# Kernel optimization log

Hardware: AMD Instinct MI355X
Metric: run time of the kernel (lower is better)

The kernel has to match this reference:

```python
import jax, jax.numpy as jnp
import numpy as np

B, N, F = 8, 1024, 256
OUT, REL = 256, 16
NADJ = 7  # ((2 relations + consecutive) * 2 for backward) + self link


def setup_inputs() -> dict:
    key = jax.random.key(0)
    k0, k1, k2, k3, k4 = jax.random.split(key, 5)
    features = jax.random.normal(k0, (B, N, F), dtype=jnp.float32)
    A1 = jax.random.uniform(k1, (B, N, N), dtype=jnp.float32)
    A2 = jax.random.uniform(k2, (B, N, N), dtype=jnp.float32)
    # learned params: one (F+REL, OUT) weight per adjacency matrix, edge embeddings init 'ones', bias (N, OUT)
    W = jax.random.normal(k3, (NADJ, F + REL, OUT), dtype=jnp.float32) * 0.05
    W_edges = jnp.ones((NADJ, REL), dtype=jnp.float32)
    b = jax.random.uniform(k4, (N, OUT), dtype=jnp.float32, minval=-0.05, maxval=0.05)
    return {"features": features, "A1": A1, "A2": A2, "W": W, "W_edges": W_edges, "b": b}


def reference(features, A1, A2, W, W_edges, b):
    # eye = A[0] * zeros(N) + eye(N)  -> batch-broadcast identity [B,N,N]
    eye = jnp.zeros_like(A1) + jnp.eye(N, dtype=A1.dtype)
    # original rolls along axis 0 (batch) of the broadcast identity (faithful replication)
    shifted = jnp.roll(eye, 1, axis=0)
    A_fwd = [A1, A2, shifted]                      # relations + consecutive link
    A_list = A_fwd + [jnp.swapaxes(a, 1, 2) for a in A_fwd]  # backward links
    A_list.append(eye)                             # self links
    A = jnp.stack(A_list, axis=0)                  # [R,B,N,N]

    # concat(features, tile(W_edges[r])) @ W[r] == features @ W[r][:F] + W_edges[r] @ W[r][F:]
    HW = jnp.einsum('bnf,rfo->rbno', features, W[:, :F]) \
         + jnp.einsum('rd,rdo->ro', W_edges, W[:, F:])[:, None, None, :]  # [R,B,N,OUT]
    AHW = jnp.einsum('rbnm,rbmo->rbno', A, HW)     # batched adjacency matmul
    out = jnp.max(AHW, axis=0) + b                 # max-aggregate over relations, add bias
    return out                                     # activation = linear
```

## Files before the change

kernel.cpp:

```cpp
#include <hip/hip_runtime.h>
#include <hip/hip_bf16.h>

#define B_ 8
#define N_ 1024
#define F_ 256
#define OUT_ 256
#define REL_ 16
#define NADJ_ 7

typedef __attribute__((ext_vector_type(8))) _Float16 f16x8;
typedef __attribute__((ext_vector_type(4))) float f32x4;

__device__ __forceinline__ void gll16(const _Float16* g, _Float16* l) {
    __builtin_amdgcn_global_load_lds(
        (const __attribute__((address_space(1))) void*)g,
        (__attribute__((address_space(3))) void*)l, 16, 0, 0);
}

__constant__ const int c_perm[7] = {0, 1, 3, 4, 2, 5, 6};

__global__ __launch_bounds__(256) void prep_kernel(const float* __restrict__ W,
                                                   const float* __restrict__ We,
                                                   const float* __restrict__ feat,
                                                   float* __restrict__ cb,
                                                   _Float16* __restrict__ WTp,
                                                   _Float16* __restrict__ Fe) {
    int bid = blockIdx.x, tid = threadIdx.x;
    if (bid < 7) {
        int idx = bid * 256 + tid;
        int j = idx / OUT_, o = idx % OUT_;
        int r = c_perm[j];
        const float* Wr = W + (size_t)r * (F_ + REL_) * OUT_;
        float s = 0.f;
#pragma unroll
        for (int d = 0; d < REL_; ++d) s += We[r * REL_ + d] * Wr[(F_ + d) * OUT_ + o];
        cb[idx] = s;
    } else if (bid < 1799) {
        int idx = (bid - 7) * 256 + tid;
        int j = idx >> 16, rem = idx & 65535, o = rem >> 8, f = rem & 255;
        int r = c_perm[j];
        WTp[idx] = (_Float16)W[((size_t)r * (F_ + REL_) + f) * OUT_ + o];
    } else {
        int i = (bid - 1799) * 256 + tid;
        size_t base = (size_t)i * 8;
        float4 a = *(const float4*)(feat + base);
        float4 b = *(const float4*)(feat + base + 4);
        f16x8 v = {(_Float16)a.x, (_Float16)a.y, (_Float16)a.z, (_Float16)a.w,
                   (_Float16)b.x, (_Float16)b.y, (_Float16)b.z, (_Float16)b.w};
        *(f16x8*)(Fe + base) = v;
    }
}

__global__ __launch_bounds__(256) void convhw_kernel(const float* __restrict__ A1,
                                                     const float* __restrict__ A2,
                                                     const _Float16* __restrict__ Fe,
                                                     const _Float16* __restrict__ WTp,
                                                     const float* __restrict__ cb,
                                                     _Float16* __restrict__ Af,
                                                     _Float16* __restrict__ HWT,
                                                     _Float16* __restrict__ HWN) {
    __shared__ _Float16 S[8192];
    const int bid = blockIdx.x, tid = threadIdx.x;
    if (bid < 896) {
        const int z = bid / 128, rem = bid % 128, bx = rem & 63, by = rem >> 6;
        const bool tr = (z < 4);
        const _Float16* A  = tr ? (WTp + (size_t)z * 65536) : Fe;
        const _Float16* Bt = tr ? Fe : (WTp + (size_t)z * 65536);
        const int m0 = (tr ? by : bx) * 128;
        const int n0 = (tr ? bx : by) * 128;
        _Float16* As = S;
        _Float16* Bs = S + 4096;
        const int wave = tid >> 6, lane = tid & 63, lm = lane & 15, q = lane >> 4;
        const int wr = (wave >> 1) * 64, wc = (wave & 1) * 64;
        const int srow = tid >> 2, sk = (tid & 3) * 8;
        const _Float16* ga0 = A + (size_t)(m0 + srow) * F_ + sk;
        const _Float16* ga1 = ga0 + (size_t)64 * F_;
        const _Float16* gb0 = Bt + (size_t)(n0 + srow) * F_ + sk;
        const _Float16* gb1 = gb0 + (size_t)64 * F_;
        _Float16* la0 = As + tid * 8;
        _Float16* la1 = As + 2048 + tid * 8;
        _Float16* lb0 = Bs + tid * 8;
        _Float16* lb1 = Bs + 2048 + tid * 8;

        f32x4 acc[4][4] = {};
        for (int k0 = 0; k0 < F_; k0 += 32) {
            gll16(ga0 + k0, la0);
            gll16(ga1 + k0, la1);
            gll16(gb0 + k0, lb0);
            gll16(gb1 + k0, lb1);
            __syncthreads();
            f16x8 af[4], bf[4];
#pragma unroll
            for (int i = 0; i < 4; ++i) af[i] = *(const f16x8*)(As + (wr + i * 16 + lm) * 32 + q * 8);
#pragma unroll
            for (int j = 0; j < 4; ++j) bf[j] = *(const f16x8*)(Bs + (wc + j * 16 + lm) * 32 + q * 8);
#pragma unroll
            for (int i = 0; i < 4; ++i)
#pragma unroll
                for (int j = 0; j < 4; ++j)
                    acc[i][j] = __builtin_amdgcn_mfma_f32_16x16x32_f16(af[i], bf[j], acc[i][j], 0, 0, 0);
            __syncthreads();
        }
        const float* cbz = cb + (size_t)z * 256;
        if (tr) {
            _Float16* C = HWT + (size_t)z * ((size_t)256 * 8192);
#pragma unroll
            for (int i = 0; i < 4; ++i)
#pragma unroll
                for (int j = 0; j < 4; ++j)
#pragma unroll
                    for (int g = 0; g < 4; ++g) {
                        int row = wr + i * 16 + q * 4 + g;
                        int col = wc + j * 16 + lm;
                        float v = acc[i][j][g] + cbz[m0 + row];
                        C[(size_t)(m0 + row) * 8192 + (n0 + col)] = (_Float16)v;
                    }
        } else {
            _Float16* C = HWN + (size_t)(z - 4) * ((size_t)8192 * 256);
#pragma unroll
            for (int i = 0; i < 4; ++i)
#pragma unroll
                for (int j = 0; j < 4; ++j)
#pragma unroll
                    for (int g = 0; g < 4; ++g) {
                        int row = wr + i * 16 + q * 4 + g;
                        int col = wc + j * 16 + lm;
                        float v = acc[i][j][g] + cbz[n0 + col];
                        C[(size_t)(m0 + row) * 256 + (n0 + col)] = (_Float16)v;
                    }
        }
    } else {
        _Float16* T = S;
        const int cbid = bid - 896;
        int z = cbid >> 8, s = z >> 3, b = z & 7;
        const float* src = (s ? A2 : A1) + (size_t)b * N_ * N_;
        int k0 = (cbid & 15) * 64, n0 = ((cbid >> 4) & 15) * 64;
        int r = tid >> 2, cs = (tid & 3) * 16;
        const float* sp = src + (size_t)(k0 + r) * N_ + n0 + cs;
        _Float16 v[16];
#pragma unroll
        for (int j = 0; j < 16; j += 4) {
            float4 f = *(const float4*)(sp + j);
            v[j] = (_Float16)f.x; v[j + 1] = (_Float16)f.y;
            v[j + 2] = (_Float16)f.z; v[j + 3] = (_Float16)f.w;
        }
        const size_t slab = (size_t)8 * N_ * N_;
#pragma unroll
        for (int j = 0; j < 16; ++j) {
            int n = cs + j;
            int sw = ((n ^ (n >> 3)) & 7) << 3;
            T[n * 64 + (r ^ sw)] = v[j];
        }
        __syncthreads();
        {
            int n = tid >> 2, i2 = (tid & 3) * 16;
            int sw = ((n ^ (n >> 3)) & 7) << 3;
            f16x8 q0 = *(const f16x8*)&T[n * 64 + (i2 ^ sw)];
            f16x8 q1 = *(const f16x8*)&T[n * 64 + ((i2 + 8) ^ sw)];
            _Float16* dt = Af + (size_t)s * slab + (size_t)b * N_ * N_ + (size_t)(n0 + n) * N_ + k0 + i2;
            *(f16x8*)dt = q0;
            *(f16x8*)(dt + 8) = q1;
        }
    }
}

__global__ __launch_bounds__(256) void p2_kernel(const float* __restrict__ A1,
                                                 const float* __restrict__ A2,
                                                 const _Float16* __restrict__ Af,
                                                 const _Float16* __restrict__ HWT,
                                                 _Float16* __restrict__ AHW) {
    __shared__ _Float16 As[128 * 32];
    __shared__ _Float16 Bs[128 * 32];
    const int d = blockIdx.x;
    const int member = (d >> 3) & 1;
    const int p = (d & 7) | ((d >> 4) << 3);
    const int mt = p & 7, zz = p >> 3;
    const int rr = zz >> 3, b = zz & 7;
    const _Float16* Bt = HWT + (size_t)rr * (256 * 8192) + (size_t)b * 1024;
    _Float16* C = AHW + (size_t)rr * (8 * 262144) + (size_t)b * 262144;
    const int m0 = mt * 128, n0 = member * 128;
    const int tid = threadIdx.x;
    const int wave = tid >> 6, lane = tid & 63, lm = lane & 15, q = lane >> 4;
    const int wr = (wave >> 1) * 64, wc = (wave & 1) * 64;
    const int srow = tid >> 2, sk = (tid & 3) * 8;
    const _Float16* gb0 = Bt + (size_t)(n0 + srow) * 8192 + sk;
    const _Float16* gb1 = gb0 + (size_t)64 * 8192;
    _Float16* la0 = As + tid * 8;
    _Float16* la1 = As + 2048 + tid * 8;
    _Float16* lb0 = Bs + tid * 8;
    _Float16* lb1 = Bs + 2048 + tid * 8;

    f32x4 acc[4][4] = {};
    if (rr < 2) {
        const float* Ag0 = ((rr & 1) ? A2 : A1) + (size_t)b * N_ * N_
                           + (size_t)(m0 + srow) * N_ + sk;
        const float* Ag1 = Ag0 + (size_t)64 * N_;
        float4 pa0 = *(const float4*)(Ag0);
        float4 pa1 = *(const float4*)(Ag0 + 4);
        float4 pb0 = *(const float4*)(Ag1);
        float4 pb1 = *(const float4*)(Ag1 + 4);
        for (int k0 = 0; k0 < N_; k0 += 32) {
            f16x8 v0 = {(_Float16)pa0.x, (_Float16)pa0.y, (_Float16)pa0.z, (_Float16)pa0.w,
                        (_Float16)pa1.x, (_Float16)pa1.y, (_Float16)pa1.z, (_Float16)pa1.w};
            f16x8 v1 = {(_Float16)pb0.x, (_Float16)pb0.y, (_Float16)pb0.z, (_Float16)pb0.w,
                        (_Float16)pb1.x, (_Float16)pb1.y, (_Float16)pb1.z, (_Float16)pb1.w};
            *(f16x8*)la0 = v0;
            *(f16x8*)la1 = v1;
            gll16(gb0 + k0, lb0);
            gll16(gb1 + k0, lb1);
            if (k0 + 32 < N_) {
                pa0 = *(const float4*)(Ag0 + k0 + 32);
                pa1 = *(const float4*)(Ag0 + k0 + 36);
                pb0 = *(const float4*)(Ag1 + k0 + 32);
                pb1 = *(const float4*)(Ag1 + k0 + 36);
            }
            __syncthreads();
            f16x8 af[4], bf[4];
#pragma unroll
            for (int i = 0; i < 4; ++i) af[i] = *(const f16x8*)(As + (wr + i * 16 + lm) * 32 + q * 8);
#pragma unroll
            for (int j = 0; j < 4; ++j) bf[j] = *(const f16x8*)(Bs + (wc + j * 16 + lm) * 32 + q * 8);
#pragma unroll
            for (int i = 0; i < 4; ++i)
#pragma unroll
                for (int j = 0; j < 4; ++j)
                    acc[i][j] = __builtin_amdgcn_mfma_f32_16x16x32_f16(af[i], bf[j], acc[i][j], 0, 0, 0);
            __syncthreads();
        }
    } else {
        const _Float16* ga0 = Af + (size_t)(rr - 2) * (8 * 1048576) + (size_t)b * 1048576
                              + (size_t)(m0 + srow) * N_ + sk;
        const _Float16* ga1 = ga0 + (size_t)64 * N_;
        for (int k0 = 0; k0 < N_; k0 += 32) {
            gll16(ga0 + k0, la0);
            gll16(ga1 + k0, la1);
            gll16(gb0 + k0, lb0);
            gll16(gb1 + k0, lb1);
            __syncthreads();
            f16x8 af[4], bf[4];
#pragma unroll
            for (int i = 0; i < 4; ++i) af[i] = *(const f16x8*)(As + (wr + i * 16 + lm) * 32 + q * 8);
#pragma unroll
            for (int j = 0; j < 4; ++j) bf[j] = *(const f16x8*)(Bs + (wc + j * 16 + lm) * 32 + q * 8);
#pragma unroll
            for (int i = 0; i < 4; ++i)
#pragma unroll
                for (int j = 0; j < 4; ++j)
                    acc[i][j] = __builtin_amdgcn_mfma_f32_16x16x32_f16(af[i], bf[j], acc[i][j], 0, 0, 0);
            __syncthreads();
        }
    }
#pragma unroll
    for (int i = 0; i < 4; ++i)
#pragma unroll
        for (int j = 0; j < 4; ++j)
#pragma unroll
            for (int g = 0; g < 4; ++g) {
                int row = wr + i * 16 + q * 4 + g;
                int col = wc + j * 16 + lm;
                C[(size_t)(m0 + row) * 256 + (n0 + col)] = (_Float16)acc[i][j][g];
            }
}

__global__ __launch_bounds__(256) void max_kernel(const _Float16* __restrict__ AHW,
                                                  const _Float16* __restrict__ HWN,
                                                  const float* __restrict__ bias,
                                                  float* __restrict__ out) {
    size_t i = ((size_t)blockIdx.x * 256 + threadIdx.x) * 8;
    const size_t slab = (size_t)B_ * N_ * OUT_;
    float m[8];
    f16x8 v = *(const f16x8*)(AHW + i);
#pragma unroll
    for (int e = 0; e < 8; ++e) m[e] = (float)v[e];
#pragma unroll
    for (int rr = 1; rr < 4; ++rr) {
        f16x8 w = *(const f16x8*)(AHW + rr * slab + i);
#pragma unroll
        for (int e = 0; e < 8; ++e) m[e] = fmaxf(m[e], (float)w[e]);
    }
#pragma unroll
    for (int j = 0; j < 3; ++j) {
        f16x8 w = *(const f16x8*)(HWN + j * slab + i);
#pragma unroll
        for (int e = 0; e < 8; ++e) m[e] = fmaxf(m[e], (float)w[e]);
    }
    size_t bidx = i & ((size_t)N_ * OUT_ - 1);
    float4 b0 = *(const float4*)(bias + bidx);
    float4 b1 = *(const float4*)(bias + bidx + 4);
    float4 o0 = {m[0] + b0.x, m[1] + b0.y, m[2] + b0.z, m[3] + b0.w};
    float4 o1 = {m[4] + b1.x, m[5] + b1.y, m[6] + b1.z, m[7] + b1.w};
    *(float4*)(out + i) = o0;
    *(float4*)(out + i + 4) = o1;
}

__global__ void cbias_kernel(const float* __restrict__ W, const float* __restrict__ We,
                             float* __restrict__ c) {
    int idx = blockIdx.x * 256 + threadIdx.x;
    if (idx >= NADJ_ * OUT_) return;
    int r = idx / OUT_, o = idx % OUT_;
    const float* Wr = W + (size_t)r * (F_ + REL_) * OUT_;
    float s = 0.f;
#pragma unroll
    for (int d = 0; d < REL_; ++d) s += We[r * REL_ + d] * Wr[(F_ + d) * OUT_ + o];
    c[idx] = s;
}

__global__ __launch_bounds__(256) void hw_kernel(const float* __restrict__ feat,
                                                 const float* __restrict__ W,
                                                 const float* __restrict__ cb,
                                                 _Float16* __restrict__ HWb) {
    __shared__ _Float16 As[64][32];
    __shared__ _Float16 Bs[64][32];
    const int mt = blockIdx.x, ct = blockIdx.y;
    const int tid = threadIdx.x, wave = tid >> 6, lane = tid & 63;
    const int r = (ct * 64) / OUT_;
    const int o0 = (ct * 64) % OUT_;
    const float* Bg = W + (size_t)r * (F_ + REL_) * OUT_ + o0;
    const int m0 = mt * 64;
    const int lm = lane & 15, q = lane >> 4;
    f32x4 acc[4] = {};
    for (int k0 = 0; k0 < F_; k0 += 32) {
        {
            int seg = (tid & 3) * 8, m = tid >> 2;
            const float* src = feat + (size_t)(m0 + m) * F_ + k0 + seg;
#pragma unroll
            for (int j = 0; j < 8; ++j) As[m][seg + j] = (_Float16)src[j];
        }
        {
            int kk = tid >> 3, ns = (tid & 7) * 8;
            const float* src = Bg + (size_t)(k0 + kk) * OUT_ + ns;
#pragma unroll
            for (int j = 0; j < 8; ++j) Bs[ns + j][kk] = (_Float16)src[j];
        }
        __syncthreads();
        f16x8 a = *(const f16x8*)&As[wave * 16 + lm][q * 8];
#pragma unroll
        for (int c4 = 0; c4 < 4; ++c4) {
            f16x8 b = *(const f16x8*)&Bs[c4 * 16 + lm][q * 8];
            acc[c4] = __builtin_amdgcn_mfma_f32_16x16x32_f16(a, b, acc[c4], 0, 0, 0);
        }
        __syncthreads();
    }
#pragma unroll
    for (int c4 = 0; c4 < 4; ++c4)
#pragma unroll
        for (int g = 0; g < 4; ++g) {
            int row = wave * 16 + (lane >> 4) * 4 + g;
            int col = c4 * 16 + lm;
            float v = acc[c4][g] + cb[r * OUT_ + o0 + col];
            HWb[((size_t)r * B_ * N_ + m0 + row) * OUT_ + o0 + col] = (_Float16)v;
        }
}

__global__ __launch_bounds__(256) void agg_kernel(const float* __restrict__ A1,
                                                  const float* __restrict__ A2,
                                                  const _Float16* __restrict__ HWb,
                                                  const float* __restrict__ bias,
                                                  float* __restrict__ out) {
    __shared__ _Float16 As[64][32];
    __shared__ _Float16 Bs[64][32];
    const int b = blockIdx.z, nt = blockIdx.y, ot = blockIdx.x;
    const int tid = threadIdx.x, wave = tid >> 6, lane = tid & 63;
    const int n0 = nt * 64, o0 = ot * 64;
    const int lm = lane & 15, q = lane >> 4;
    const size_t rstride = (size_t)B_ * N_ * OUT_;
    f32x4 mx[4];
#pragma unroll
    for (int i = 0; i < 4; ++i) mx[i] = f32x4{-1e30f, -1e30f, -1e30f, -1e30f};
#pragma unroll 1
    for (int rr = 0; rr < 4; ++rr) {
        const float* Ag = ((rr & 1) ? A2 : A1) + (size_t)b * N_ * N_;
        const bool tr = (rr >= 2);
        const int r = (rr < 2) ? rr : rr + 1;
        const _Float16* Bg = HWb + (size_t)r * rstride + (size_t)b * N_ * OUT_ + o0;
        f32x4 acc[4] = {};
        for (int k0 = 0; k0 < N_; k0 += 32) {
            if (!tr) {
                int seg = (tid & 3) * 8, m = tid >> 2;
                const float* src = Ag + (size_t)(n0 + m) * N_ + k0 + seg;
#pragma unroll
                for (int j = 0; j < 8; ++j) As[m][seg + j] = (_Float16)src[j];
            } else {
                int kk = tid >> 3, ms = (tid & 7) * 8;
                const float* src = Ag + (size_t)(k0 + kk) * N_ + n0 + ms;
#pragma unroll
                for (int j = 0; j < 8; ++j) As[ms + j][kk] = (_Float16)src[j];
            }
            {
                int kk = tid >> 3, ns = (tid & 7) * 8;
                const _Float16* src = Bg + (size_t)(k0 + kk) * OUT_ + ns;
#pragma unroll
                for (int j = 0; j < 8; ++j) Bs[ns + j][kk] = src[j];
            }
            __syncthreads();
            f16x8 a = *(const f16x8*)&As[wave * 16 + lm][q * 8];
#pragma unroll
            for (int c4 = 0; c4 < 4; ++c4) {
                f16x8 bb = *(const f16x8*)&Bs[c4 * 16 + lm][q * 8];
                acc[c4] = __builtin_amdgcn_mfma_f32_16x16x32_f16(a, bb, acc[c4], 0, 0, 0);
            }
            __syncthreads();
        }
#pragma unroll
        for (int c4 = 0; c4 < 4; ++c4)
#pragma unroll
            for (int g = 0; g < 4; ++g) mx[c4][g] = fmaxf(mx[c4][g], acc[c4][g]);
    }
#pragma unroll
    for (int c4 = 0; c4 < 4; ++c4)
#pragma unroll
        for (int g = 0; g < 4; ++g) {
            int row = wave * 16 + (lane >> 4) * 4 + g;
            int col = c4 * 16 + lm;
            size_t pos = ((size_t)b * N_ + n0 + row) * OUT_ + o0 + col;
            float v = mx[c4][g];
            v = fmaxf(v, (float)HWb[2 * rstride + pos]);
            v = fmaxf(v, (float)HWb[5 * rstride + pos]);
            v = fmaxf(v, (float)HWb[6 * rstride + pos]);
            out[pos] = v + bias[((size_t)(n0 + row)) * OUT_ + o0 + col];
        }
}

extern "C" void kernel_launch(void* const* d_in, const int* in_sizes, int n_in,
                              void* d_out, int out_size, void* d_ws, size_t ws_size,
                              hipStream_t stream) {
    const float* feat = (const float*)d_in[0];
    const float* A1   = (const float*)d_in[1];
    const float* A2   = (const float*)d_in[2];
    const float* W    = (const float*)d_in[3];
    const float* We   = (const float*)d_in[4];
    const float* bias = (const float*)d_in[5];
    float* out = (float*)d_out;

    const size_t OFF_CB   = 0;
    const size_t OFF_WT   = 8192;
    const size_t OFF_FE   = 1048576;
    const size_t OFF_AF   = 5242880;
    const size_t OFF_HWT  = 72351744;
    const size_t OFF_HWN  = 89128960;
    const size_t OFF_AHW  = 101711872;
    const size_t WS_NEEDED = 118489088;

    if (ws_size >= WS_NEEDED) {
        float*    cbp = (float*)((char*)d_ws + OFF_CB);
        _Float16* WTp = (_Float16*)((char*)d_ws + OFF_WT);
        _Float16* Fe  = (_Float16*)((char*)d_ws + OFF_FE);
        _Float16* Af  = (_Float16*)((char*)d_ws + OFF_AF);
        _Float16* HWT = (_Float16*)((char*)d_ws + OFF_HWT);
        _Float16* HWN = (_Float16*)((char*)d_ws + OFF_HWN);
        _Float16* AHW = (_Float16*)((char*)d_ws + OFF_AHW);

        prep_kernel<<<2823, 256, 0, stream>>>(W, We, feat, cbp, WTp, Fe);
        convhw_kernel<<<4992, 256, 0, stream>>>(A1, A2, Fe, WTp, cbp, Af, HWT, HWN);
        p2_kernel<<<512, 256, 0, stream>>>(A1, A2, Af, HWT, AHW);
        max_kernel<<<1024, 256, 0, stream>>>(AHW, HWN, bias, out);
    } else {
        float* cb = (float*)d_ws;
        _Float16* HWb = (_Float16*)((char*)d_ws + 8192);
        cbias_kernel<<<7, 256, 0, stream>>>(W, We, cb);
        hw_kernel<<<dim3(128, 28), 256, 0, stream>>>(feat, W, cb, HWb);
        agg_kernel<<<dim3(4, 16, 8), 256, 0, stream>>>(A1, A2, HWb, bias, out);
    }
}
```

Before: 176.4 us.

## Fuse A transpose-to-fp16 into aggregation GEMM, dropping Af staging buffer

Removes the separate pass that converted A1/A2 to fp16 and transposed them into a workspace buffer. The aggregation kernel now reads fp32 A directly, transposes it on the fly into an XOR-swizzled shared-memory tile, and prefetches the next k-slice into registers. The forward-A path gets the same swizzle. This avoids writing and re-reading 32 MB of fp16 A. In exchange, the transposed reads are fp32 and column-strided, and each output tile re-reads and re-converts A instead of reading pre-converted fp16.

```diff
diff --git a/kernel.cpp b/kernel.cpp
--- a/kernel.cpp
+++ b/kernel.cpp
@@ -9,6 +9,7 @@
 #define NADJ_ 7
 
 typedef __attribute__((ext_vector_type(8))) _Float16 f16x8;
+typedef __attribute__((ext_vector_type(2))) _Float16 f16x2;
 typedef __attribute__((ext_vector_type(4))) float f32x4;
 
 __device__ __forceinline__ void gll16(const _Float16* g, _Float16* l) {
@@ -51,122 +52,83 @@
     }
 }
 
-__global__ __launch_bounds__(256) void convhw_kernel(const float* __restrict__ A1,
-                                                     const float* __restrict__ A2,
-                                                     const _Float16* __restrict__ Fe,
-                                                     const _Float16* __restrict__ WTp,
-                                                     const float* __restrict__ cb,
-                                                     _Float16* __restrict__ Af,
-                                                     _Float16* __restrict__ HWT,
-                                                     _Float16* __restrict__ HWN) {
-    __shared__ _Float16 S[8192];
-    const int bid = blockIdx.x, tid = threadIdx.x;
-    if (bid < 896) {
-        const int z = bid / 128, rem = bid % 128, bx = rem & 63, by = rem >> 6;
-        const bool tr = (z < 4);
-        const _Float16* A  = tr ? (WTp + (size_t)z * 65536) : Fe;
-        const _Float16* Bt = tr ? Fe : (WTp + (size_t)z * 65536);
-        const int m0 = (tr ? by : bx) * 128;
-        const int n0 = (tr ? bx : by) * 128;
-        _Float16* As = S;
-        _Float16* Bs = S + 4096;
-        const int wave = tid >> 6, lane = tid & 63, lm = lane & 15, q = lane >> 4;
-        const int wr = (wave >> 1) * 64, wc = (wave & 1) * 64;
-        const int srow = tid >> 2, sk = (tid & 3) * 8;
-        const _Float16* ga0 = A + (size_t)(m0 + srow) * F_ + sk;
-        const _Float16* ga1 = ga0 + (size_t)64 * F_;
-        const _Float16* gb0 = Bt + (size_t)(n0 + srow) * F_ + sk;
-        const _Float16* gb1 = gb0 + (size_t)64 * F_;
-        _Float16* la0 = As + tid * 8;
-        _Float16* la1 = As + 2048 + tid * 8;
-        _Float16* lb0 = Bs + tid * 8;
-        _Float16* lb1 = Bs + 2048 + tid * 8;
-
-        f32x4 acc[4][4] = {};
-        for (int k0 = 0; k0 < F_; k0 += 32) {
-            gll16(ga0 + k0, la0);
-            gll16(ga1 + k0, la1);
-            gll16(gb0 + k0, lb0);
-            gll16(gb1 + k0, lb1);
-            __syncthreads();
-            f16x8 af[4], bf[4];
-#pragma unroll
-            for (int i = 0; i < 4; ++i) af[i] = *(const f16x8*)(As + (wr + i * 16 + lm) * 32 + q * 8);
-#pragma unroll
-            for (int j = 0; j < 4; ++j) bf[j] = *(const f16x8*)(Bs + (wc + j * 16 + lm) * 32 + q * 8);
-#pragma unroll
-            for (int i = 0; i < 4; ++i)
-#pragma unroll
-                for (int j = 0; j < 4; ++j)
-                    acc[i][j] = __builtin_amdgcn_mfma_f32_16x16x32_f16(af[i], bf[j], acc[i][j], 0, 0, 0);
-            __syncthreads();
-        }
-        const float* cbz = cb + (size_t)z * 256;
-        if (tr) {
-            _Float16* C = HWT + (size_t)z * ((size_t)256 * 8192);
-#pragma unroll
-            for (int i = 0; i < 4; ++i)
-#pragma unroll
-                for (int j = 0; j < 4; ++j)
-#pragma unroll
-                    for (int g = 0; g < 4; ++g) {
-                        int row = wr + i * 16 + q * 4 + g;
-                        int col = wc + j * 16 + lm;
-                        float v = acc[i][j][g] + cbz[m0 + row];
-                        C[(size_t)(m0 + row) * 8192 + (n0 + col)] = (_Float16)v;
-                    }
-        } else {
-            _Float16* C = HWN + (size_t)(z - 4) * ((size_t)8192 * 256);
-#pragma unroll
-            for (int i = 0; i < 4; ++i)
-#pragma unroll
-                for (int j = 0; j < 4; ++j)
-#pragma unroll
-                    for (int g = 0; g < 4; ++g) {
-                        int row = wr + i * 16 + q * 4 + g;
-                        int col = wc + j * 16 + lm;
-                        float v = acc[i][j][g] + cbz[n0 + col];
-                        C[(size_t)(m0 + row) * 256 + (n0 + col)] = (_Float16)v;
-                    }
-        }
+__global__ __launch_bounds__(256) void hw7_kernel(const _Float16* __restrict__ Fe,
+                                                  const _Float16* __restrict__ WTp,
+                                                  const float* __restrict__ cb,
+                                                  _Float16* __restrict__ HWT,
+                                                  _Float16* __restrict__ HWN) {
+    __shared__ _Float16 As[128 * 32];
+    __shared__ _Float16 Bs[128 * 32];
+    const int z = blockIdx.z, bx = blockIdx.x, by = blockIdx.y;
+    const bool tr = (z < 4);
+    const _Float16* A  = tr ? (WTp + (size_t)z * 65536) : Fe;
+    const _Float16* Bt = tr ? Fe : (WTp + (size_t)z * 65536);
+    const int m0 = (tr ? by : bx) * 128;
+    const int n0 = (tr ? bx : by) * 128;
+    const int tid = threadIdx.x;
+    const int wave = tid >> 6, lane = tid & 63, lm = lane & 15, q = lane >> 4;
+    const int wr = (wave >> 1) * 64, wc = (wave & 1) * 64;
+    const int srow = tid >> 2, sk = (tid & 3) * 8;
+    const _Float16* ga0 = A + (size_t)(m0 + srow) * F_ + sk;
+    const _Float16* ga1 = ga0 + (size_t)64 * F_;
+    const _Float16* gb0 = Bt + (size_t)(n0 + srow) * F_ + sk;
+    const _Float16* gb1 = gb0 + (size_t)64 * F_;
+    _Float16* la0 = As + tid * 8;
+    _Float16* la1 = As + 2048 + tid * 8;
+    _Float16* lb0 = Bs + tid * 8;
+    _Float16* lb1 = Bs + 2048 + tid * 8;
+
+    f32x4 acc[4][4] = {};
+    for (int k0 = 0; k0 < F_; k0 += 32) {
+        gll16(ga0 + k0, la0);
+        gll16(ga1 + k0, la1);
+        gll16(gb0 + k0, lb0);
+        gll16(gb1 + k0, lb1);
+        __syncthreads();
+        f16x8 af[4], bf[4];
+#pragma unroll
+        for (int i = 0; i < 4; ++i) af[i] = *(const f16x8*)(As + (wr + i * 16 + lm) * 32 + q * 8);
+#pragma unroll
+        for (int j = 0; j < 4; ++j) bf[j] = *(const f16x8*)(Bs + (wc + j * 16 + lm) * 32 + q * 8);
+#pragma unroll
+        for (int i = 0; i < 4; ++i)
+#pragma unroll
+            for (int j = 0; j < 4; ++j)
+                acc[i][j] = __builtin_amdgcn_mfma_f32_16x16x32_f16(af[i], bf[j], acc[i][j], 0, 0, 0);
+        __syncthreads();
+    }
+    const float* cbz = cb + (size_t)z * 256;
+    if (tr) {
+        _Float16* C = HWT + (size_t)z * ((size_t)256 * 8192);
+#pragma unroll
+        for (int i = 0; i < 4; ++i)
+#pragma unroll
+            for (int j = 0; j < 4; ++j)
+#pragma unroll
+                for (int g = 0; g < 4; ++g) {
+                    int row = wr + i * 16 + q * 4 + g;
+                    int col = wc + j * 16 + lm;
+                    float v = acc[i][j][g] + cbz[m0 + row];
+                    C[(size_t)(m0 + row) * 8192 + (n0 + col)] = (_Float16)v;
+                }
     } else {
-        _Float16* T = S;
-        const int cbid = bid - 896;
-        int z = cbid >> 8, s = z >> 3, b = z & 7;
-        const float* src = (s ? A2 : A1) + (size_t)b * N_ * N_;
-        int k0 = (cbid & 15) * 64, n0 = ((cbid >> 4) & 15) * 64;
-        int r = tid >> 2, cs = (tid & 3) * 16;
-        const float* sp = src + (size_t)(k0 + r) * N_ + n0 + cs;
-        _Float16 v[16];
-#pragma unroll
-        for (int j = 0; j < 16; j += 4) {
-            float4 f = *(const float4*)(sp + j);
-            v[j] = (_Float16)f.x; v[j + 1] = (_Float16)f.y;
-            v[j + 2] = (_Float16)f.z; v[j + 3] = (_Float16)f.w;
-        }
-        const size_t slab = (size_t)8 * N_ * N_;
-#pragma unroll
-        for (int j = 0; j < 16; ++j) {
-            int n = cs + j;
-            int sw = ((n ^ (n >> 3)) & 7) << 3;
-            T[n * 64 + (r ^ sw)] = v[j];
-        }
-        __syncthreads();
-        {
-            int n = tid >> 2, i2 = (tid & 3) * 16;
-            int sw = ((n ^ (n >> 3)) & 7) << 3;
-            f16x8 q0 = *(const f16x8*)&T[n * 64 + (i2 ^ sw)];
-            f16x8 q1 = *(const f16x8*)&T[n * 64 + ((i2 + 8) ^ sw)];
-            _Float16* dt = Af + (size_t)s * slab + (size_t)b * N_ * N_ + (size_t)(n0 + n) * N_ + k0 + i2;
-            *(f16x8*)dt = q0;
-            *(f16x8*)(dt + 8) = q1;
-        }
+        _Float16* C = HWN + (size_t)(z - 4) * ((size_t)8192 * 256);
+#pragma unroll
+        for (int i = 0; i < 4; ++i)
+#pragma unroll
+            for (int j = 0; j < 4; ++j)
+#pragma unroll
+                for (int g = 0; g < 4; ++g) {
+                    int row = wr + i * 16 + q * 4 + g;
+                    int col = wc + j * 16 + lm;
+                    float v = acc[i][j][g] + cbz[n0 + col];
+                    C[(size_t)(m0 + row) * 256 + (n0 + col)] = (_Float16)v;
+                }
     }
 }
 
 __global__ __launch_bounds__(256) void p2_kernel(const float* __restrict__ A1,
                                                  const float* __restrict__ A2,
-                                                 const _Float16* __restrict__ Af,
                                                  const _Float16* __restrict__ HWT,
                                                  _Float16* __restrict__ AHW) {
     __shared__ _Float16 As[128 * 32];
@@ -185,15 +147,16 @@
     const int srow = tid >> 2, sk = (tid & 3) * 8;
     const _Float16* gb0 = Bt + (size_t)(n0 + srow) * 8192 + sk;
     const _Float16* gb1 = gb0 + (size_t)64 * 8192;
-    _Float16* la0 = As + tid * 8;
-    _Float16* la1 = As + 2048 + tid * 8;
     _Float16* lb0 = Bs + tid * 8;
     _Float16* lb1 = Bs + 2048 + tid * 8;
-
+    const int swA = (q * 8) ^ ((lm & 3) << 3);
+
+    const float* Ag = ((rr & 1) ? A2 : A1) + (size_t)b * N_ * N_;
     f32x4 acc[4][4] = {};
     if (rr < 2) {
-        const float* Ag0 = ((rr & 1) ? A2 : A1) + (size_t)b * N_ * N_
-                           + (size_t)(m0 + srow) * N_ + sk;
+        _Float16* la0 = As + srow * 32 + (sk ^ ((srow & 3) << 3));
+        _Float16* la1 = la0 + 64 * 32;
+        const float* Ag0 = Ag + (size_t)(m0 + srow) * N_ + sk;
         const float* Ag1 = Ag0 + (size_t)64 * N_;
         float4 pa0 = *(const float4*)(Ag0);
         float4 pa1 = *(const float4*)(Ag0 + 4);
@@ -217,9 +180,11 @@
             __syncthreads();
             f16x8 af[4], bf[4];
 #pragma unroll
-            for (int i = 0; i < 4; ++i) af[i] = *(const f16x8*)(As + (wr + i * 16 + lm) * 32 + q * 8);
-#pragma unroll
-            for (int j = 0; j < 4; ++j) bf[j] = *(const f16x8*)(Bs + (wc + j * 16 + lm) * 32 + q * 8);
+            for (int i = 0; i < 4; ++i)
+                af[i] = *(const f16x8*)(As + (wr + i * 16 + lm) * 32 + swA);
+#pragma unroll
+            for (int j = 0; j < 4; ++j)
+                bf[j] = *(const f16x8*)(Bs + (wc + j * 16 + lm) * 32 + q * 8);
 #pragma unroll
             for (int i = 0; i < 4; ++i)
 #pragma unroll
@@ -228,20 +193,37 @@
             __syncthreads();
         }
     } else {
-        const _Float16* ga0 = Af + (size_t)(rr - 2) * (8 * 1048576) + (size_t)b * 1048576
-                              + (size_t)(m0 + srow) * N_ + sk;
-        const _Float16* ga1 = ga0 + (size_t)64 * N_;
+        const int kk2 = (tid & 15) * 2, ns = (tid >> 4) * 8;
+        const float* Ar0 = Ag + (size_t)kk2 * N_ + m0 + ns;
+        float4 f00 = *(const float4*)(Ar0);
+        float4 f01 = *(const float4*)(Ar0 + 4);
+        float4 f10 = *(const float4*)(Ar0 + N_);
+        float4 f11 = *(const float4*)(Ar0 + N_ + 4);
         for (int k0 = 0; k0 < N_; k0 += 32) {
-            gll16(ga0 + k0, la0);
-            gll16(ga1 + k0, la1);
+            float fa[8] = {f00.x, f00.y, f00.z, f00.w, f01.x, f01.y, f01.z, f01.w};
+            float fb[8] = {f10.x, f10.y, f10.z, f10.w, f11.x, f11.y, f11.z, f11.w};
+#pragma unroll
+            for (int j = 0; j < 8; ++j) {
+                f16x2 v2 = {(_Float16)fa[j], (_Float16)fb[j]};
+                *(f16x2*)(As + (ns + j) * 32 + (kk2 ^ ((j & 3) << 3))) = v2;
+            }
             gll16(gb0 + k0, lb0);
             gll16(gb1 + k0, lb1);
+            if (k0 + 32 < N_) {
+                const float* nx = Ar0 + (size_t)(k0 + 32) * N_;
+                f00 = *(const float4*)(nx);
+                f01 = *(const float4*)(nx + 4);
+                f10 = *(const float4*)(nx + N_);
+                f11 = *(const float4*)(nx + N_ + 4);
+            }
             __syncthreads();
             f16x8 af[4], bf[4];
 #pragma unroll
-            for (int i = 0; i < 4; ++i) af[i] = *(const f16x8*)(As + (wr + i * 16 + lm) * 32 + q * 8);
-#pragma unroll
-            for (int j = 0; j < 4; ++j) bf[j] = *(const f16x8*)(Bs + (wc + j * 16 + lm) * 32 + q * 8);
+            for (int i = 0; i < 4; ++i)
+                af[i] = *(const f16x8*)(As + (wr + i * 16 + lm) * 32 + swA);
+#pragma unroll
+            for (int j = 0; j < 4; ++j)
+                bf[j] = *(const f16x8*)(Bs + (wc + j * 16 + lm) * 32 + q * 8);
 #pragma unroll
             for (int i = 0; i < 4; ++i)
 #pragma unroll
@@ -435,7 +417,6 @@
     const size_t OFF_CB   = 0;
     const size_t OFF_WT   = 8192;
     const size_t OFF_FE   = 1048576;
-    const size_t OFF_AF   = 5242880;
     const size_t OFF_HWT  = 72351744;
     const size_t OFF_HWN  = 89128960;
     const size_t OFF_AHW  = 101711872;
@@ -445,14 +426,13 @@
         float*    cbp = (float*)((char*)d_ws + OFF_CB);
         _Float16* WTp = (_Float16*)((char*)d_ws + OFF_WT);
         _Float16* Fe  = (_Float16*)((char*)d_ws + OFF_FE);
-        _Float16* Af  = (_Float16*)((char*)d_ws + OFF_AF);
         _Float16* HWT = (_Float16*)((char*)d_ws + OFF_HWT);
         _Float16* HWN = (_Float16*)((char*)d_ws + OFF_HWN);
         _Float16* AHW = (_Float16*)((char*)d_ws + OFF_AHW);
 
         prep_kernel<<<2823, 256, 0, stream>>>(W, We, feat, cbp, WTp, Fe);
-        convhw_kernel<<<4992, 256, 0, stream>>>(A1, A2, Fe, WTp, cbp, Af, HWT, HWN);
-        p2_kernel<<<512, 256, 0, stream>>>(A1, A2, Af, HWT, AHW);
+        hw7_kernel<<<dim3(64, 2, 7), 256, 0, stream>>>(Fe, WTp, cbp, HWT, HWN);
+        p2_kernel<<<512, 256, 0, stream>>>(A1, A2, HWT, AHW);
         max_kernel<<<1024, 256, 0, stream>>>(AHW, HWN, bias, out);
     } else {
         float* cb = (float*)d_ws;
```

Result: slower. 195.5 us (+10.9%).
